# Optimization experiments

Measured on AMD Instinct MI355X. Metric: run time of the kernel, lower is better.

The kernel has to match this reference:

```python
import jax, jax.numpy as jnp
import numpy as np
from jax import lax

D_MODEL, D_STATE, D_CONV, EXPAND = 512, 16, 4, 2
D_INNER = EXPAND * D_MODEL          # 1024
DT_RANK = (D_MODEL + 15) // 16      # 32
BATCH, SEQ = 4, 1024


def setup_inputs() -> dict:
    key = jax.random.key(0)
    ks = jax.random.split(key, 8)
    s = 0.02
    x = jax.random.normal(ks[0], (BATCH, SEQ, D_MODEL), jnp.float32)
    in_proj_w = jax.random.normal(ks[1], (2 * D_INNER, D_MODEL), jnp.float32) * s
    conv_w = jax.random.normal(ks[2], (D_INNER, 1, D_CONV), jnp.float32) * s  # depthwise
    conv_b = jnp.zeros((D_INNER,), jnp.float32)
    x_proj_w = jax.random.normal(ks[3], (DT_RANK + 2 * D_STATE, D_INNER), jnp.float32) * s
    dt_proj_w = jax.random.normal(ks[4], (D_INNER, DT_RANK), jnp.float32) * s
    dt_proj_b = jax.random.normal(ks[5], (D_INNER,), jnp.float32) * 0.1
    # Mamba S4D-real init: A = -[1..d_state] per channel, stored as log
    A_log = jnp.log(jnp.tile(jnp.arange(1, D_STATE + 1, dtype=jnp.float32)[None, :], (D_INNER, 1)))
    D = jnp.ones((D_INNER,), jnp.float32)
    out_proj_w = jax.random.normal(ks[6], (D_MODEL, D_INNER), jnp.float32) * s
    ln_w = jnp.ones((D_MODEL,), jnp.float32)
    ln_b = jnp.zeros((D_MODEL,), jnp.float32)
    return dict(x=x, in_proj_w=in_proj_w, conv_w=conv_w, conv_b=conv_b,
                x_proj_w=x_proj_w, dt_proj_w=dt_proj_w, dt_proj_b=dt_proj_b,
                A_log=A_log, D=D, out_proj_w=out_proj_w, ln_w=ln_w, ln_b=ln_b)


def _selective_scan(u, delta, A, Bm, Cm, D):
    # u, delta: (B,L,Di); A: (Di,N); Bm, Cm: (B,L,N)
    dA = jnp.exp(delta[..., None] * A)                    # (B,L,Di,N)
    dBu = (delta * u)[..., None] * Bm[:, :, None, :]      # (B,L,Di,N)
    dA_t = jnp.moveaxis(dA, 1, 0)                         # (L,B,Di,N)
    dBu_t = jnp.moveaxis(dBu, 1, 0)
    C_t = jnp.moveaxis(Cm, 1, 0)                          # (L,B,N)

    def step(h, inp):
        dA_i, dBu_i, C_i = inp
        h = dA_i * h + dBu_i                              # (B,Di,N)
        y = jnp.einsum('bdn,bn->bd', h, C_i)
        return h, y

    h0 = jnp.zeros((u.shape[0], A.shape[0], A.shape[1]), u.dtype)
    _, ys = lax.scan(step, h0, (dA_t, dBu_t, C_t))        # ys: (L,B,Di)
    return jnp.moveaxis(ys, 0, 1) + u * D                 # (B,L,Di)


def reference(x, in_proj_w, conv_w, conv_b, x_proj_w, dt_proj_w, dt_proj_b,
              A_log, D, out_proj_w, ln_w, ln_b):
    # ---- Mamba SSM ----
    xz = jnp.einsum('bld,ed->ble', x, in_proj_w)          # (B,L,2*Di)
    xs, z = jnp.split(xz, 2, axis=-1)
    # causal depthwise conv over time
    xt = jnp.moveaxis(xs, 1, 2)                           # (B,Di,L)
    xt = lax.conv_general_dilated(xt, conv_w, window_strides=(1,),
                                  padding=[(D_CONV - 1, 0)],
                                  feature_group_count=D_INNER,
                                  dimension_numbers=('NCH', 'OIH', 'NCH'))
    xt = xt + conv_b[None, :, None]
    u = jax.nn.silu(jnp.moveaxis(xt, 1, 2))               # (B,L,Di)

    x_dbl = jnp.einsum('bld,ed->ble', u, x_proj_w)        # (B,L,dt_rank+2N)
    dt = x_dbl[..., :DT_RANK]
    Bm = x_dbl[..., DT_RANK:DT_RANK + D_STATE]
    Cm = x_dbl[..., DT_RANK + D_STATE:]
    delta = jax.nn.softplus(jnp.einsum('blr,dr->bld', dt, dt_proj_w) + dt_proj_b)
    A = -jnp.exp(A_log)                                   # (Di,N)

    y = _selective_scan(u, delta, A, Bm, Cm, D)
    y = y * jax.nn.silu(z)
    ssm_out = jnp.einsum('ble,de->bld', y, out_proj_w)    # (B,L,Dm)

    # ---- residual + LayerNorm ----
    r = x + ssm_out
    mu = jnp.mean(r, axis=-1, keepdims=True)
    var = jnp.mean(jnp.square(r - mu), axis=-1, keepdims=True)
    return (r - mu) / jnp.sqrt(var + 1e-5) * ln_w + ln_b
```

## Files before the change

kernel.cpp:

```cpp
#include <hip/hip_runtime.h>
#include <hip/hip_bf16.h>
#include <math.h>

#define B_   4
#define L_   1024
#define DM   512
#define DI   1024
#define NS   16
#define XDC  64
#define BL   4096
#define KS   4
#define CL   256
#define BCS  258

typedef short bfrag __attribute__((ext_vector_type(8)));
typedef float ffrag __attribute__((ext_vector_type(4)));

__device__ __forceinline__ ushort f2bf(float v) {
    __hip_bfloat16 h = __float2bfloat16(v);
    return *(ushort*)&h;
}

template<bool F32>
__device__ __forceinline__ void stage8(const void* p, size_t eoff, ushort* dst) {
    if constexpr (F32) {
        const float* f = (const float*)p + eoff;
        float4 v0 = *(const float4*)f;
        float4 v1 = *(const float4*)(f + 4);
        *(ushort4*)dst       = make_ushort4(f2bf(v0.x), f2bf(v0.y), f2bf(v0.z), f2bf(v0.w));
        *(ushort4*)(dst + 4) = make_ushort4(f2bf(v1.x), f2bf(v1.y), f2bf(v1.z), f2bf(v1.w));
    } else {
        *(uint4*)dst = *(const uint4*)((const ushort*)p + eoff);
    }
}

template<int EPI, bool AF, bool BF>
__global__ __launch_bounds__(256) void gemm_mfma(const void* __restrict__ Ap,
        const void* __restrict__ Bp, float* __restrict__ C,
        int K, int ldc, const float* __restrict__ resid)
{
    __shared__ ushort As[128][40];
    __shared__ ushort Bs[128][40];
    const int tid = threadIdx.x;
    const int lane = tid & 63, wave = tid >> 6;
    const int wm = (wave & 1) * 64, wn = (wave >> 1) * 64;
    const int l15 = lane & 15, quad = lane >> 4;
    const int m0 = blockIdx.y * 128, n0 = blockIdx.x * 128;

    ffrag acc[4][4] = {};

    for (int k0 = 0; k0 < K; k0 += 32) {
        #pragma unroll
        for (int i = 0; i < 2; i++) {
            int chunk = tid + i * 256;
            int row = chunk >> 2, kk8 = (chunk & 3) * 8;
            stage8<AF>(Ap, (size_t)(m0 + row) * K + k0 + kk8, &As[row][kk8]);
            stage8<BF>(Bp, (size_t)(n0 + row) * K + k0 + kk8, &Bs[row][kk8]);
        }
        __syncthreads();
        bfrag af[4], bfv[4];
        #pragma unroll
        for (int i = 0; i < 4; i++) {
            af[i]  = *(const bfrag*)&As[wm + i * 16 + l15][quad * 8];
            bfv[i] = *(const bfrag*)&Bs[wn + i * 16 + l15][quad * 8];
        }
        #pragma unroll
        for (int i = 0; i < 4; i++)
            #pragma unroll
            for (int j = 0; j < 4; j++)
                acc[i][j] = __builtin_amdgcn_mfma_f32_16x16x32_bf16(af[i], bfv[j], acc[i][j], 0, 0, 0);
        __syncthreads();
    }

    #pragma unroll
    for (int i = 0; i < 4; i++) {
        #pragma unroll
        for (int j = 0; j < 4; j++) {
            int n = n0 + wn + j * 16 + l15;
            #pragma unroll
            for (int r = 0; r < 4; r++) {
                int m = m0 + wm + i * 16 + quad * 4 + r;
                float v = acc[i][j][r];
                if (EPI == 2) v += resid[(size_t)m * ldc + n];
                C[(size_t)m * ldc + n] = v;
            }
        }
    }
}

__global__ __launch_bounds__(256) void gemm3_splitk(const float* __restrict__ uT,
        const float* __restrict__ xw, float* __restrict__ part)
{
    __shared__ float As[16][33];
    __shared__ float Ws[16][68];
    const int tid = threadIdx.x;
    const int tx = tid & 15, ty = tid >> 4;
    const int ks = blockIdx.x, m0 = blockIdx.y * 32;
    const int kbase = ks * (DI / KS);
    float acc[2][4] = {};

    for (int k0 = 0; k0 < DI / KS; k0 += 16) {
        if (tid < 128) {
            int k = tid >> 3, m4 = (tid & 7) * 4;
            const float4 v = *(const float4*)&uT[(size_t)(kbase + k0 + k) * BL + m0 + m4];
            As[k][m4 + 0] = v.x; As[k][m4 + 1] = v.y;
            As[k][m4 + 2] = v.z; As[k][m4 + 3] = v.w;
        }
        {
            int r = tid >> 2, c4 = (tid & 3) * 4;
            const float4 v = *(const float4*)&xw[(size_t)r * DI + kbase + k0 + c4];
            Ws[c4 + 0][r] = v.x; Ws[c4 + 1][r] = v.y;
            Ws[c4 + 2][r] = v.z; Ws[c4 + 3][r] = v.w;
        }
        __syncthreads();
        #pragma unroll
        for (int kk = 0; kk < 16; kk++) {
            float a[2], b[4];
            a[0] = As[kk][ty * 2 + 0];
            a[1] = As[kk][ty * 2 + 1];
            #pragma unroll
            for (int j = 0; j < 4; j++) b[j] = Ws[kk][tx * 4 + j];
            #pragma unroll
            for (int i = 0; i < 2; i++)
                #pragma unroll
                for (int j = 0; j < 4; j++)
                    acc[i][j] = fmaf(a[i], b[j], acc[i][j]);
        }
        __syncthreads();
    }

    float* pp = part + (size_t)ks * BL * XDC;
    #pragma unroll
    for (int i = 0; i < 2; i++) {
        int m = m0 + ty * 2 + i;
        *(float4*)&pp[(size_t)m * XDC + tx * 4] =
            make_float4(acc[i][0], acc[i][1], acc[i][2], acc[i][3]);
    }
}

__global__ __launch_bounds__(256) void gemm3_reduce(const float* __restrict__ part,
        float* __restrict__ xdbl)
{
    int i = blockIdx.x * 256 + threadIdx.x;
    const float4* p0 = (const float4*)part;
    float4 a = p0[i];
    #pragma unroll
    for (int s = 1; s < KS; s++) {
        float4 b = p0[i + (size_t)s * BL * XDC / 4];
        a.x += b.x; a.y += b.y; a.z += b.z; a.w += b.w;
    }
    ((float4*)xdbl)[i] = a;
}

__global__ __launch_bounds__(256) void dt_softplus(const float* __restrict__ xdbl,
        const float* __restrict__ dtw, const float* __restrict__ bias,
        float* __restrict__ deltaT)
{
    __shared__ float dts[256][33];
    const int tid = threadIdx.x;
    const int lane = tid & 63;
    const int bl0 = blockIdx.x * 256;

    {
        const float4* src = (const float4*)(xdbl + (size_t)(bl0 + tid) * XDC);
        #pragma unroll
        for (int k = 0; k < 8; k++) {
            float4 v = src[k];
            *(float4*)&dts[tid][k * 4] = v;
        }
    }

    int d = blockIdx.y * 4 + (tid >> 6);
    d = __builtin_amdgcn_readfirstlane(d);
    float wreg[32];
    {
        const float4* wp = (const float4*)(dtw + (size_t)d * 32);
        #pragma unroll
        for (int k = 0; k < 8; k++) *(float4*)&wreg[k * 4] = wp[k];
    }
    const float bb = bias[d];
    __syncthreads();

    #pragma unroll
    for (int s = 0; s < 4; s++) {
        const int bl = s * 64 + lane;
        float acc = bb;
        #pragma unroll
        for (int k = 0; k < 8; k++) {
            float4 v = *(const float4*)&dts[bl][k * 4];
            acc = fmaf(wreg[k * 4 + 0], v.x, acc);
            acc = fmaf(wreg[k * 4 + 1], v.y, acc);
            acc = fmaf(wreg[k * 4 + 2], v.z, acc);
            acc = fmaf(wreg[k * 4 + 3], v.w, acc);
        }
        float outv = (acc > 20.f) ? acc : __logf(1.f + __expf(acc));
        deltaT[(size_t)d * BL + bl0 + bl] = outv;
    }
}

__global__ __launch_bounds__(256) void conv_silu(const float* __restrict__ xzT,
        const float* __restrict__ cw, const float* __restrict__ cb,
        float* __restrict__ uT)
{
    int i = blockIdx.x * 256 + threadIdx.x;
    int d  = i >> 10;
    int q  = i & 1023;
    int bl = q * 4;
    int l  = bl & (L_ - 1);
    const float* row = xzT + (size_t)d * BL;
    float4 cur = *(const float4*)&row[bl];
    float4 prev = make_float4(0.f, 0.f, 0.f, 0.f);
    if (l != 0) prev = *(const float4*)&row[bl - 4];
    float v[7] = { prev.y, prev.z, prev.w, cur.x, cur.y, cur.z, cur.w };
    float w0 = cw[d * 4 + 0], w1 = cw[d * 4 + 1], w2 = cw[d * 4 + 2], w3 = cw[d * 4 + 3];
    float bias = cb[d];
    float4 o;
    o.x = bias + w0 * v[0] + w1 * v[1] + w2 * v[2] + w3 * v[3];
    o.y = bias + w0 * v[1] + w1 * v[2] + w2 * v[3] + w3 * v[4];
    o.z = bias + w0 * v[2] + w1 * v[3] + w2 * v[4] + w3 * v[5];
    o.w = bias + w0 * v[3] + w1 * v[4] + w2 * v[5] + w3 * v[6];
    o.x = o.x / (1.f + __expf(-o.x));
    o.y = o.y / (1.f + __expf(-o.y));
    o.z = o.z / (1.f + __expf(-o.z));
    o.w = o.w / (1.f + __expf(-o.w));
    *(float4*)&uT[(size_t)d * BL + bl] = o;
}

__global__ __launch_bounds__(512) void scan_fused(const float* __restrict__ deltaT,
        const float* __restrict__ uT, const float* __restrict__ xdbl,
        const float* __restrict__ xzT, const float* __restrict__ A_log,
        const float* __restrict__ Dp, float* __restrict__ yT)
{
    __shared__ float bc[32 * BCS];

    const int tid = threadIdx.x;
    const int lane = tid & 63;
    const int bd = blockIdx.x * 8 + (tid >> 6);
    const int d = bd & (DI - 1);
    const int b = bd >> 10;

    float Acoef[16];
    {
        const float4* ap = (const float4*)(A_log + d * NS);
        #pragma unroll
        for (int i = 0; i < 4; i++) {
            float4 v = ap[i];
            Acoef[i * 4 + 0] = -__expf(v.x); Acoef[i * 4 + 1] = -__expf(v.y);
            Acoef[i * 4 + 2] = -__expf(v.z); Acoef[i * 4 + 3] = -__expf(v.w);
        }
    }
    const float Dd = Dp[d];

    const size_t row_t = (size_t)d * BL + b * L_;
    const size_t row_z = (size_t)(DI + d) * BL + b * L_;

    float h[16];
    #pragma unroll
    for (int n = 0; n < 16; n++) h[n] = 0.f;

    for (int c = 0; c < L_ / CL; c++) {
        __syncthreads();
        {
            const float* src = xdbl + ((size_t)b * L_ + c * CL) * XDC + 32;
            #pragma unroll
            for (int i = 0; i < 4; i++) {
                int idx = tid + i * 512;
                int l = idx >> 3, c4 = idx & 7;
                float4 v = *(const float4*)&src[(size_t)l * XDC + c4 * 4];
                int n0 = c4 * 4;
                bc[(n0 + 0) * BCS + l] = v.x;
                bc[(n0 + 1) * BCS + l] = v.y;
                bc[(n0 + 2) * BCS + l] = v.z;
                bc[(n0 + 3) * BCS + l] = v.w;
            }
        }
        __syncthreads();

        const int l0 = c * CL + lane * 4;
        const int lb = lane * 4;
        float4 dvv = *(const float4*)&deltaT[row_t + l0];
        float4 uvv = *(const float4*)&uT[row_t + l0];
        float dv[4] = { dvv.x, dvv.y, dvv.z, dvv.w };
        float du[4] = { dvv.x * uvv.x, dvv.y * uvv.y, dvv.z * uvv.z, dvv.w * uvv.w };
        float sa = dv[0] + dv[1] + dv[2] + dv[3];

        float a[16], bb[16];
        #pragma unroll
        for (int n = 0; n < 16; n++) {
            a[n] = __expf(sa * Acoef[n]);
            const float4 Bv = *(const float4*)&bc[n * BCS + lb];
            float acc = du[0] * Bv.x;
            acc = fmaf(__expf(dv[1] * Acoef[n]), acc, du[1] * Bv.y);
            acc = fmaf(__expf(dv[2] * Acoef[n]), acc, du[2] * Bv.z);
            acc = fmaf(__expf(dv[3] * Acoef[n]), acc, du[3] * Bv.w);
            bb[n] = acc;
        }

        #pragma unroll
        for (int off = 1; off < 64; off <<= 1) {
            #pragma unroll
            for (int n = 0; n < 16; n++) {
                float pa = __shfl_up(a[n], off);
                float pb = __shfl_up(bb[n], off);
                if (lane >= off) {
                    bb[n] = fmaf(a[n], pb, bb[n]);
                    a[n] *= pa;
                }
            }
        }

        #pragma unroll
        for (int n = 0; n < 16; n++) {
            float pa = __shfl_up(a[n], 1);
            float pb = __shfl_up(bb[n], 1);
            float ae = (lane == 0) ? 1.f : pa;
            float be = (lane == 0) ? 0.f : pb;
            h[n] = fmaf(ae, h[n], be);
        }

        float s0 = 0.f, s1 = 0.f, s2 = 0.f, s3 = 0.f;
        #pragma unroll
        for (int n = 0; n < 16; n++) {
            const float4 Bv = *(const float4*)&bc[n * BCS + lb];
            const float4 Cv = *(const float4*)&bc[(16 + n) * BCS + lb];
            float hn = h[n];
            hn = fmaf(__expf(dv[0] * Acoef[n]), hn, du[0] * Bv.x);
            s0 = fmaf(hn, Cv.x, s0);
            hn = fmaf(__expf(dv[1] * Acoef[n]), hn, du[1] * Bv.y);
            s1 = fmaf(hn, Cv.y, s1);
            hn = fmaf(__expf(dv[2] * Acoef[n]), hn, du[2] * Bv.z);
            s2 = fmaf(hn, Cv.z, s2);
            hn = fmaf(__expf(dv[3] * Acoef[n]), hn, du[3] * Bv.w);
            s3 = fmaf(hn, Cv.w, s3);
            h[n] = hn;
        }

        #pragma unroll
        for (int n = 0; n < 16; n++) h[n] = __shfl(h[n], 63);

        float4 zv = *(const float4*)&xzT[row_z + l0];
        float4 yv;
        float v0 = s0 + uvv.x * Dd; yv.x = v0 * (zv.x / (1.f + __expf(-zv.x)));
        float v1 = s1 + uvv.y * Dd; yv.y = v1 * (zv.y / (1.f + __expf(-zv.y)));
        float v2 = s2 + uvv.z * Dd; yv.z = v2 * (zv.z / (1.f + __expf(-zv.z)));
        float v3 = s3 + uvv.w * Dd; yv.w = v3 * (zv.w / (1.f + __expf(-zv.w)));
        *(float4*)&yT[row_t + l0] = yv;
    }
}

__global__ __launch_bounds__(256) void transpose_cast(const float* __restrict__ yT,
        ushort* __restrict__ yB)
{
    __shared__ float t[64][65];
    const int bl0 = blockIdx.x * 64, d0 = blockIdx.y * 64;
    const int tid = threadIdx.x;
    #pragma unroll
    for (int i = 0; i < 4; i++) {
        int chunk = tid + i * 256;
        int dr = chunk >> 4, c4 = (chunk & 15) * 4;
        const float4 v = *(const float4*)&yT[(size_t)(d0 + dr) * BL + bl0 + c4];
        t[dr][c4 + 0] = v.x; t[dr][c4 + 1] = v.y;
        t[dr][c4 + 2] = v.z; t[dr][c4 + 3] = v.w;
    }
    __syncthreads();
    #pragma unroll
    for (int i = 0; i < 4; i++) {
        int chunk = tid + i * 256;
        int br = chunk >> 4, dc4 = (chunk & 15) * 4;
        ushort4 o;
        o.x = f2bf(t[dc4 + 0][br]); o.y = f2bf(t[dc4 + 1][br]);
        o.z = f2bf(t[dc4 + 2][br]); o.w = f2bf(t[dc4 + 3][br]);
        *(ushort4*)&yB[(size_t)(bl0 + br) * DI + d0 + dc4] = o;
    }
}

__global__ __launch_bounds__(256) void ln_kernel(const float* __restrict__ r,
        const float* __restrict__ lnw, const float* __restrict__ lnb,
        float* __restrict__ out)
{
    int row = blockIdx.x;
    const float* rr = r + (size_t)row * DM;
    float v0 = rr[threadIdx.x], v1 = rr[threadIdx.x + 256];
    float s = v0 + v1, s2 = v0 * v0 + v1 * v1;
    #pragma unroll
    for (int off = 32; off > 0; off >>= 1) {
        s  += __shfl_down(s, off);
        s2 += __shfl_down(s2, off);
    }
    __shared__ float ls[4], ls2[4];
    __shared__ float mu_s, rstd_s;
    int wid = threadIdx.x >> 6, lane = threadIdx.x & 63;
    if (lane == 0) { ls[wid] = s; ls2[wid] = s2; }
    __syncthreads();
    if (threadIdx.x == 0) {
        float S = ls[0] + ls[1] + ls[2] + ls[3];
        float S2 = ls2[0] + ls2[1] + ls2[2] + ls2[3];
        float mu = S * (1.f / DM);
        float var = S2 * (1.f / DM) - mu * mu;
        mu_s = mu;
        rstd_s = rsqrtf(var + 1e-5f);
    }
    __syncthreads();
    float mu = mu_s, rstd = rstd_s;
    out[(size_t)row * DM + threadIdx.x] =
        (v0 - mu) * rstd * lnw[threadIdx.x] + lnb[threadIdx.x];
    out[(size_t)row * DM + threadIdx.x + 256] =
        (v1 - mu) * rstd * lnw[threadIdx.x + 256] + lnb[threadIdx.x + 256];
}

extern "C" void kernel_launch(void* const* d_in, const int* in_sizes, int n_in,
                              void* d_out, int out_size, void* d_ws, size_t ws_size,
                              hipStream_t stream)
{
    const float* x         = (const float*)d_in[0];
    const float* in_proj_w = (const float*)d_in[1];
    const float* conv_w    = (const float*)d_in[2];
    const float* conv_b    = (const float*)d_in[3];
    const float* x_proj_w  = (const float*)d_in[4];
    const float* dt_proj_w = (const float*)d_in[5];
    const float* dt_proj_b = (const float*)d_in[6];
    const float* A_log     = (const float*)d_in[7];
    const float* Dvec      = (const float*)d_in[8];
    const float* out_proj_w= (const float*)d_in[9];
    const float* ln_w      = (const float*)d_in[10];
    const float* ln_b      = (const float*)d_in[11];
    float* out = (float*)d_out;

    float* ws     = (float*)d_ws;
    float* xzT    = ws;
    float* uT     = xzT    + (size_t)2048 * BL;
    float* xdbl   = uT     + (size_t)DI * BL;
    float* deltaT = xdbl   + (size_t)BL * XDC;
    float* yT     = deltaT + (size_t)DI * BL;
    float* r      = yT     + (size_t)DI * BL;
    float*  xdblp = yT;
    ushort* yB    = (ushort*)deltaT;

    dim3 blk(256);

    gemm_mfma<0, true, true><<<dim3(BL / 128, 2048 / 128), blk, 0, stream>>>(
        in_proj_w, x, xzT, DM, BL, nullptr);

    conv_silu<<<(DI * BL / 4) / 256, blk, 0, stream>>>(xzT, conv_w, conv_b, uT);

    gemm3_splitk<<<dim3(KS, BL / 32), blk, 0, stream>>>(uT, x_proj_w, xdblp);
    gemm3_reduce<<<(BL * XDC / 4) / 256, blk, 0, stream>>>(xdblp, xdbl);

    dt_softplus<<<dim3(BL / 256, DI / 4), blk, 0, stream>>>(
        xdbl, dt_proj_w, dt_proj_b, deltaT);

    scan_fused<<<B_ * DI / 8, dim3(512), 0, stream>>>(
        deltaT, uT, xdbl, xzT, A_log, Dvec, yT);

    transpose_cast<<<dim3(BL / 64, DI / 64), blk, 0, stream>>>(yT, yB);

    gemm_mfma<2, false, true><<<dim3(DM / 128, BL / 128), blk, 0, stream>>>(
        yB, out_proj_w, r, DI, DM, x);

    ln_kernel<<<BL, blk, 0, stream>>>(r, ln_w, ln_b, out);
}
```

Before: 275.1 us.

## Fuse dt projection and bf16 transpose-cast into the selective scan kernel

```diff
diff --git a/kernel.cpp b/kernel.cpp
--- a/kernel.cpp
+++ b/kernel.cpp
@@ -150,52 +150,6 @@
         a.x += b.x; a.y += b.y; a.z += b.z; a.w += b.w;
     }
     ((float4*)xdbl)[i] = a;
-}
-
-__global__ __launch_bounds__(256) void dt_softplus(const float* __restrict__ xdbl,
-        const float* __restrict__ dtw, const float* __restrict__ bias,
-        float* __restrict__ deltaT)
-{
-    __shared__ float dts[256][33];
-    const int tid = threadIdx.x;
-    const int lane = tid & 63;
-    const int bl0 = blockIdx.x * 256;
-
-    {
-        const float4* src = (const float4*)(xdbl + (size_t)(bl0 + tid) * XDC);
-        #pragma unroll
-        for (int k = 0; k < 8; k++) {
-            float4 v = src[k];
-            *(float4*)&dts[tid][k * 4] = v;
-        }
-    }
-
-    int d = blockIdx.y * 4 + (tid >> 6);
-    d = __builtin_amdgcn_readfirstlane(d);
-    float wreg[32];
-    {
-        const float4* wp = (const float4*)(dtw + (size_t)d * 32);
-        #pragma unroll
-        for (int k = 0; k < 8; k++) *(float4*)&wreg[k * 4] = wp[k];
-    }
-    const float bb = bias[d];
-    __syncthreads();
-
-    #pragma unroll
-    for (int s = 0; s < 4; s++) {
-        const int bl = s * 64 + lane;
-        float acc = bb;
-        #pragma unroll
-        for (int k = 0; k < 8; k++) {
-            float4 v = *(const float4*)&dts[bl][k * 4];
-            acc = fmaf(wreg[k * 4 + 0], v.x, acc);
-            acc = fmaf(wreg[k * 4 + 1], v.y, acc);
-            acc = fmaf(wreg[k * 4 + 2], v.z, acc);
-            acc = fmaf(wreg[k * 4 + 3], v.w, acc);
-        }
-        float outv = (acc > 20.f) ? acc : __logf(1.f + __expf(acc));
-        deltaT[(size_t)d * BL + bl0 + bl] = outv;
-    }
 }
 
 __global__ __launch_bounds__(256) void conv_silu(const float* __restrict__ xzT,
@@ -226,18 +180,22 @@
     *(float4*)&uT[(size_t)d * BL + bl] = o;
 }
 
-__global__ __launch_bounds__(512) void scan_fused(const float* __restrict__ deltaT,
-        const float* __restrict__ uT, const float* __restrict__ xdbl,
-        const float* __restrict__ xzT, const float* __restrict__ A_log,
-        const float* __restrict__ Dp, float* __restrict__ yT)
+__global__ __launch_bounds__(512) void scan_fused(const float* __restrict__ uT,
+        const float* __restrict__ xdbl, const float* __restrict__ xzT,
+        const float* __restrict__ A_log, const float* __restrict__ Dp,
+        const float* __restrict__ dtw, const float* __restrict__ dtb,
+        ushort* __restrict__ yB)
 {
     __shared__ float bc[32 * BCS];
+    __shared__ float ys[8][CL + 4];
 
     const int tid = threadIdx.x;
     const int lane = tid & 63;
-    const int bd = blockIdx.x * 8 + (tid >> 6);
-    const int d = bd & (DI - 1);
-    const int b = bd >> 10;
+    const int w = tid >> 6;
+    const int bd0 = blockIdx.x * 8;
+    const int d0 = bd0 & (DI - 1);
+    const int b = bd0 >> 10;
+    const int d = d0 + w;
 
     float Acoef[16];
     {
@@ -250,6 +208,15 @@
         }
     }
     const float Dd = Dp[d];
+
+    const int d_u = __builtin_amdgcn_readfirstlane(d);
+    float wreg[32];
+    {
+        const float4* wp = (const float4*)(dtw + (size_t)d_u * 32);
+        #pragma unroll
+        for (int k = 0; k < 8; k++) *(float4*)&wreg[k * 4] = wp[k];
+    }
+    const float dbias = dtb[d_u];
 
     const size_t row_t = (size_t)d * BL + b * L_;
     const size_t row_z = (size_t)(DI + d) * BL + b * L_;
@@ -278,10 +245,28 @@
 
         const int l0 = c * CL + lane * 4;
         const int lb = lane * 4;
-        float4 dvv = *(const float4*)&deltaT[row_t + l0];
+
+        float dv[4];
+        {
+            const float* dtrow = xdbl + (size_t)(b * L_ + l0) * XDC;
+            #pragma unroll
+            for (int j = 0; j < 4; j++) {
+                const float4* rp = (const float4*)(dtrow + (size_t)j * XDC);
+                float acc = dbias;
+                #pragma unroll
+                for (int k = 0; k < 8; k++) {
+                    float4 v = rp[k];
+                    acc = fmaf(wreg[k * 4 + 0], v.x, acc);
+                    acc = fmaf(wreg[k * 4 + 1], v.y, acc);
+                    acc = fmaf(wreg[k * 4 + 2], v.z, acc);
+                    acc = fmaf(wreg[k * 4 + 3], v.w, acc);
+                }
+                dv[j] = (acc > 20.f) ? acc : __logf(1.f + __expf(acc));
+            }
+        }
+
         float4 uvv = *(const float4*)&uT[row_t + l0];
-        float dv[4] = { dvv.x, dvv.y, dvv.z, dvv.w };
-        float du[4] = { dvv.x * uvv.x, dvv.y * uvv.y, dvv.z * uvv.z, dvv.w * uvv.w };
+        float du[4] = { dv[0] * uvv.x, dv[1] * uvv.y, dv[2] * uvv.z, dv[3] * uvv.w };
         float sa = dv[0] + dv[1] + dv[2] + dv[3];
 
         float a[16], bb[16];
@@ -344,33 +329,17 @@
         float v1 = s1 + uvv.y * Dd; yv.y = v1 * (zv.y / (1.f + __expf(-zv.y)));
         float v2 = s2 + uvv.z * Dd; yv.z = v2 * (zv.z / (1.f + __expf(-zv.z)));
         float v3 = s3 + uvv.w * Dd; yv.w = v3 * (zv.w / (1.f + __expf(-zv.w)));
-        *(float4*)&yT[row_t + l0] = yv;
-    }
-}
-
-__global__ __launch_bounds__(256) void transpose_cast(const float* __restrict__ yT,
-        ushort* __restrict__ yB)
-{
-    __shared__ float t[64][65];
-    const int bl0 = blockIdx.x * 64, d0 = blockIdx.y * 64;
-    const int tid = threadIdx.x;
-    #pragma unroll
-    for (int i = 0; i < 4; i++) {
-        int chunk = tid + i * 256;
-        int dr = chunk >> 4, c4 = (chunk & 15) * 4;
-        const float4 v = *(const float4*)&yT[(size_t)(d0 + dr) * BL + bl0 + c4];
-        t[dr][c4 + 0] = v.x; t[dr][c4 + 1] = v.y;
-        t[dr][c4 + 2] = v.z; t[dr][c4 + 3] = v.w;
-    }
-    __syncthreads();
-    #pragma unroll
-    for (int i = 0; i < 4; i++) {
-        int chunk = tid + i * 256;
-        int br = chunk >> 4, dc4 = (chunk & 15) * 4;
-        ushort4 o;
-        o.x = f2bf(t[dc4 + 0][br]); o.y = f2bf(t[dc4 + 1][br]);
-        o.z = f2bf(t[dc4 + 2][br]); o.w = f2bf(t[dc4 + 3][br]);
-        *(ushort4*)&yB[(size_t)(bl0 + br) * DI + d0 + dc4] = o;
+        *(float4*)&ys[w][lb] = yv;
+        __syncthreads();
+
+        if (tid < CL) {
+            int l = tid;
+            ushort os[8];
+            #pragma unroll
+            for (int k = 0; k < 8; k++) os[k] = f2bf(ys[k][l]);
+            size_t bl = (size_t)b * L_ + c * CL + l;
+            *(uint4*)&yB[bl * DI + d0] = *(uint4*)os;
+        }
     }
 }
 
@@ -428,13 +397,11 @@
 
     float* ws     = (float*)d_ws;
     float* xzT    = ws;
-    float* uT     = xzT    + (size_t)2048 * BL;
-    float* xdbl   = uT     + (size_t)DI * BL;
-    float* deltaT = xdbl   + (size_t)BL * XDC;
-    float* yT     = deltaT + (size_t)DI * BL;
-    float* r      = yT     + (size_t)DI * BL;
-    float*  xdblp = yT;
-    ushort* yB    = (ushort*)deltaT;
+    float* uT     = xzT  + (size_t)2048 * BL;
+    float* xdbl   = uT   + (size_t)DI * BL;
+    ushort* yB    = (ushort*)(xdbl + (size_t)BL * XDC);
+    float* r      = (float*)((char*)yB + (size_t)BL * DI * 2);
+    float* xdblp  = r;
 
     dim3 blk(256);
 
@@ -446,13 +413,8 @@
     gemm3_splitk<<<dim3(KS, BL / 32), blk, 0, stream>>>(uT, x_proj_w, xdblp);
     gemm3_reduce<<<(BL * XDC / 4) / 256, blk, 0, stream>>>(xdblp, xdbl);
 
-    dt_softplus<<<dim3(BL / 256, DI / 4), blk, 0, stream>>>(
-        xdbl, dt_proj_w, dt_proj_b, deltaT);
-
     scan_fused<<<B_ * DI / 8, dim3(512), 0, stream>>>(
-        deltaT, uT, xdbl, xzT, A_log, Dvec, yT);
-
-    transpose_cast<<<dim3(BL / 64, DI / 64), blk, 0, stream>>>(yT, yB);
+        uT, xdbl, xzT, A_log, Dvec, dt_proj_w, dt_proj_b, yB);
 
     gemm_mfma<2, false, true><<<dim3(DM / 128, BL / 128), blk, 0, stream>>>(
         yB, out_proj_w, r, DI, DM, x);
```

After: 298.9 us. 1.09x slower.

## Store x_proj output transposed so scan reads B/C directly without LDS staging

Applied to the files above, without the earlier changes.

```diff
diff --git a/kernel.cpp b/kernel.cpp
--- a/kernel.cpp
+++ b/kernel.cpp
@@ -11,7 +11,6 @@
 #define BL   4096
 #define KS   4
 #define CL   256
-#define BCS  258
 
 typedef short bfrag __attribute__((ext_vector_type(8)));
 typedef float ffrag __attribute__((ext_vector_type(4)));
@@ -94,10 +93,11 @@
     __shared__ float As[16][33];
     __shared__ float Ws[16][68];
     const int tid = threadIdx.x;
-    const int tx = tid & 15, ty = tid >> 4;
+    const int nn = tid & 63;
+    const int mg = tid >> 6;
     const int ks = blockIdx.x, m0 = blockIdx.y * 32;
     const int kbase = ks * (DI / KS);
-    float acc[2][4] = {};
+    float acc[8] = {};
 
     for (int k0 = 0; k0 < DI / KS; k0 += 16) {
         if (tid < 128) {
@@ -115,60 +115,40 @@
         __syncthreads();
         #pragma unroll
         for (int kk = 0; kk < 16; kk++) {
-            float a[2], b[4];
-            a[0] = As[kk][ty * 2 + 0];
-            a[1] = As[kk][ty * 2 + 1];
+            float w = Ws[kk][nn];
             #pragma unroll
-            for (int j = 0; j < 4; j++) b[j] = Ws[kk][tx * 4 + j];
-            #pragma unroll
-            for (int i = 0; i < 2; i++)
-                #pragma unroll
-                for (int j = 0; j < 4; j++)
-                    acc[i][j] = fmaf(a[i], b[j], acc[i][j]);
+            for (int i = 0; i < 8; i++)
+                acc[i] = fmaf(As[kk][mg * 8 + i], w, acc[i]);
         }
         __syncthreads();
     }
 
-    float* pp = part + (size_t)ks * BL * XDC;
-    #pragma unroll
-    for (int i = 0; i < 2; i++) {
-        int m = m0 + ty * 2 + i;
-        *(float4*)&pp[(size_t)m * XDC + tx * 4] =
-            make_float4(acc[i][0], acc[i][1], acc[i][2], acc[i][3]);
-    }
+    float* pp = part + (size_t)ks * 64 * BL + (size_t)nn * BL + m0 + mg * 8;
+    *(float4*)&pp[0] = make_float4(acc[0], acc[1], acc[2], acc[3]);
+    *(float4*)&pp[4] = make_float4(acc[4], acc[5], acc[6], acc[7]);
 }
 
 __global__ __launch_bounds__(256) void gemm3_reduce(const float* __restrict__ part,
-        float* __restrict__ xdbl)
+        float* __restrict__ xdblT)
 {
     int i = blockIdx.x * 256 + threadIdx.x;
     const float4* p0 = (const float4*)part;
     float4 a = p0[i];
     #pragma unroll
     for (int s = 1; s < KS; s++) {
-        float4 b = p0[i + (size_t)s * BL * XDC / 4];
+        float4 b = p0[i + (size_t)s * 64 * BL / 4];
         a.x += b.x; a.y += b.y; a.z += b.z; a.w += b.w;
     }
-    ((float4*)xdbl)[i] = a;
-}
-
-__global__ __launch_bounds__(256) void dt_softplus(const float* __restrict__ xdbl,
+    ((float4*)xdblT)[i] = a;
+}
+
+__global__ __launch_bounds__(256) void dt_softplus(const float* __restrict__ xdblT,
         const float* __restrict__ dtw, const float* __restrict__ bias,
         float* __restrict__ deltaT)
 {
-    __shared__ float dts[256][33];
     const int tid = threadIdx.x;
     const int lane = tid & 63;
-    const int bl0 = blockIdx.x * 256;
-
-    {
-        const float4* src = (const float4*)(xdbl + (size_t)(bl0 + tid) * XDC);
-        #pragma unroll
-        for (int k = 0; k < 8; k++) {
-            float4 v = src[k];
-            *(float4*)&dts[tid][k * 4] = v;
-        }
-    }
+    const int bl = blockIdx.x * 256 + lane * 4;
 
     int d = blockIdx.y * 4 + (tid >> 6);
     d = __builtin_amdgcn_readfirstlane(d);
@@ -179,23 +159,23 @@
         for (int k = 0; k < 8; k++) *(float4*)&wreg[k * 4] = wp[k];
     }
     const float bb = bias[d];
-    __syncthreads();
-
-    #pragma unroll
-    for (int s = 0; s < 4; s++) {
-        const int bl = s * 64 + lane;
-        float acc = bb;
-        #pragma unroll
-        for (int k = 0; k < 8; k++) {
-            float4 v = *(const float4*)&dts[bl][k * 4];
-            acc = fmaf(wreg[k * 4 + 0], v.x, acc);
-            acc = fmaf(wreg[k * 4 + 1], v.y, acc);
-            acc = fmaf(wreg[k * 4 + 2], v.z, acc);
-            acc = fmaf(wreg[k * 4 + 3], v.w, acc);
-        }
-        float outv = (acc > 20.f) ? acc : __logf(1.f + __expf(acc));
-        deltaT[(size_t)d * BL + bl0 + bl] = outv;
-    }
+
+    float4 acc = make_float4(bb, bb, bb, bb);
+    #pragma unroll
+    for (int k = 0; k < 32; k++) {
+        float4 v = *(const float4*)&xdblT[(size_t)k * BL + bl];
+        float w = wreg[k];
+        acc.x = fmaf(w, v.x, acc.x);
+        acc.y = fmaf(w, v.y, acc.y);
+        acc.z = fmaf(w, v.z, acc.z);
+        acc.w = fmaf(w, v.w, acc.w);
+    }
+    float4 o;
+    o.x = (acc.x > 20.f) ? acc.x : __logf(1.f + __expf(acc.x));
+    o.y = (acc.y > 20.f) ? acc.y : __logf(1.f + __expf(acc.y));
+    o.z = (acc.z > 20.f) ? acc.z : __logf(1.f + __expf(acc.z));
+    o.w = (acc.w > 20.f) ? acc.w : __logf(1.f + __expf(acc.w));
+    *(float4*)&deltaT[(size_t)d * BL + bl] = o;
 }
 
 __global__ __launch_bounds__(256) void conv_silu(const float* __restrict__ xzT,
@@ -226,16 +206,14 @@
     *(float4*)&uT[(size_t)d * BL + bl] = o;
 }
 
-__global__ __launch_bounds__(512) void scan_fused(const float* __restrict__ deltaT,
-        const float* __restrict__ uT, const float* __restrict__ xdbl,
+__global__ __launch_bounds__(256) void scan_fused(const float* __restrict__ deltaT,
+        const float* __restrict__ uT, const float* __restrict__ xdblT,
         const float* __restrict__ xzT, const float* __restrict__ A_log,
         const float* __restrict__ Dp, float* __restrict__ yT)
 {
-    __shared__ float bc[32 * BCS];
-
     const int tid = threadIdx.x;
     const int lane = tid & 63;
-    const int bd = blockIdx.x * 8 + (tid >> 6);
+    const int bd = blockIdx.x * 4 + (tid >> 6);
     const int d = bd & (DI - 1);
     const int b = bd >> 10;
 
@@ -253,31 +231,16 @@
 
     const size_t row_t = (size_t)d * BL + b * L_;
     const size_t row_z = (size_t)(DI + d) * BL + b * L_;
+    const float* xB = xdblT + (size_t)32 * BL + b * L_;
+    const float* xC = xdblT + (size_t)48 * BL + b * L_;
 
     float h[16];
     #pragma unroll
     for (int n = 0; n < 16; n++) h[n] = 0.f;
 
     for (int c = 0; c < L_ / CL; c++) {
-        __syncthreads();
-        {
-            const float* src = xdbl + ((size_t)b * L_ + c * CL) * XDC + 32;
-            #pragma unroll
-            for (int i = 0; i < 4; i++) {
-                int idx = tid + i * 512;
-                int l = idx >> 3, c4 = idx & 7;
-                float4 v = *(const float4*)&src[(size_t)l * XDC + c4 * 4];
-                int n0 = c4 * 4;
-                bc[(n0 + 0) * BCS + l] = v.x;
-                bc[(n0 + 1) * BCS + l] = v.y;
-                bc[(n0 + 2) * BCS + l] = v.z;
-                bc[(n0 + 3) * BCS + l] = v.w;
-            }
-        }
-        __syncthreads();
-
         const int l0 = c * CL + lane * 4;
-        const int lb = lane * 4;
+
         float4 dvv = *(const float4*)&deltaT[row_t + l0];
         float4 uvv = *(const float4*)&uT[row_t + l0];
         float dv[4] = { dvv.x, dvv.y, dvv.z, dvv.w };
@@ -288,7 +251,7 @@
         #pragma unroll
         for (int n = 0; n < 16; n++) {
             a[n] = __expf(sa * Acoef[n]);
-            const float4 Bv = *(const float4*)&bc[n * BCS + lb];
+            const float4 Bv = *(const float4*)&xB[(size_t)n * BL + l0];
             float acc = du[0] * Bv.x;
             acc = fmaf(__expf(dv[1] * Acoef[n]), acc, du[1] * Bv.y);
             acc = fmaf(__expf(dv[2] * Acoef[n]), acc, du[2] * Bv.z);
@@ -321,8 +284,8 @@
         float s0 = 0.f, s1 = 0.f, s2 = 0.f, s3 = 0.f;
         #pragma unroll
         for (int n = 0; n < 16; n++) {
-            const float4 Bv = *(const float4*)&bc[n * BCS + lb];
-            const float4 Cv = *(const float4*)&bc[(16 + n) * BCS + lb];
+            const float4 Bv = *(const float4*)&xB[(size_t)n * BL + l0];
+            const float4 Cv = *(const float4*)&xC[(size_t)n * BL + l0];
             float hn = h[n];
             hn = fmaf(__expf(dv[0] * Acoef[n]), hn, du[0] * Bv.x);
             s0 = fmaf(hn, Cv.x, s0);
@@ -429,8 +392,8 @@
     float* ws     = (float*)d_ws;
     float* xzT    = ws;
     float* uT     = xzT    + (size_t)2048 * BL;
-    float* xdbl   = uT     + (size_t)DI * BL;
-    float* deltaT = xdbl   + (size_t)BL * XDC;
+    float* xdblT  = uT     + (size_t)DI * BL;
+    float* deltaT = xdblT  + (size_t)XDC * BL;
     float* yT     = deltaT + (size_t)DI * BL;
     float* r      = yT     + (size_t)DI * BL;
     float*  xdblp = yT;
@@ -444,13 +407,13 @@
     conv_silu<<<(DI * BL / 4) / 256, blk, 0, stream>>>(xzT, conv_w, conv_b, uT);
 
     gemm3_splitk<<<dim3(KS, BL / 32), blk, 0, stream>>>(uT, x_proj_w, xdblp);
-    gemm3_reduce<<<(BL * XDC / 4) / 256, blk, 0, stream>>>(xdblp, xdbl);
+    gemm3_reduce<<<(64 * BL / 4) / 256, blk, 0, stream>>>(xdblp, xdblT);
 
     dt_softplus<<<dim3(BL / 256, DI / 4), blk, 0, stream>>>(
-        xdbl, dt_proj_w, dt_proj_b, deltaT);
-
-    scan_fused<<<B_ * DI / 8, dim3(512), 0, stream>>>(
-        deltaT, uT, xdbl, xzT, A_log, Dvec, yT);
+        xdblT, dt_proj_w, dt_proj_b, deltaT);
+
+    scan_fused<<<B_ * DI / 4, blk, 0, stream>>>(
+        deltaT, uT, xdblT, xzT, A_log, Dvec, yT);
 
     transpose_cast<<<dim3(BL / 64, DI / 64), blk, 0, stream>>>(yT, yB);
 
```

After: 278.1 us. Within noise of the previous version (+1.1%).
